# Kernel tuning notes

Measured on AMD Instinct MI355X. Metric: run time of the kernel, lower is better.

The kernel has to match this reference:

```python
import jax, jax.numpy as jnp
import numpy as np

N_NODES = 50000
N_EDGES = 800000
D = 128
BN_EPS = 1e-5


def setup_inputs() -> dict:
    key = jax.random.key(0)
    ks = jax.random.split(key, 8)
    scale = 1.0 / np.sqrt(D)
    return {
        "nfeat": jax.random.normal(ks[0], (N_NODES, D), dtype=jnp.float32),
        "efeat": jax.random.normal(ks[1], (N_EDGES, D), dtype=jnp.float32),
        "src": jax.random.randint(ks[2], (N_EDGES,), 0, N_NODES, dtype=jnp.int32),
        "dst": jax.random.randint(ks[3], (N_EDGES,), 0, N_NODES, dtype=jnp.int32),
        "W1": jax.random.normal(ks[4], (D, D), dtype=jnp.float32) * scale,
        "b1": jnp.zeros((D,), dtype=jnp.float32),
        "gamma": jnp.ones((D,), dtype=jnp.float32),
        "beta": jnp.zeros((D,), dtype=jnp.float32),
        "W2": jax.random.normal(ks[5], (D, D), dtype=jnp.float32) * scale,
        "b2": jnp.zeros((D,), dtype=jnp.float32),
        "We": jax.random.normal(ks[6], (D, D), dtype=jnp.float32) * scale,
        "be": jnp.zeros((D,), dtype=jnp.float32),
    }


def reference(nfeat, efeat, src, dst, W1, b1, gamma, beta, W2, b2, We, be):
    n = nfeat.shape[0]
    # GINConv, sum aggregator, eps=0: h = (1+eps)*x + sum_{j in N(i)} x_j
    agg = jax.ops.segment_sum(nfeat[src], dst, num_segments=n)  # [N, D]
    h = nfeat + agg
    # apply_func: Linear -> BatchNorm1d (training-mode batch stats) -> ReLU -> Linear
    h = h @ W1 + b1
    mu = jnp.mean(h, axis=0)
    var = jnp.mean(jnp.square(h - mu), axis=0)  # biased variance, as BatchNorm uses
    h = gamma * (h - mu) * jax.lax.rsqrt(var + BN_EPS) + beta
    h = jax.nn.relu(h)
    h = h @ W2 + b2
    # edge branch: linear on edge feats, scatter-sum to destination nodes, residual add
    e = efeat @ We + be                                          # [E, D]
    h_e = jax.ops.segment_sum(e, dst, num_segments=n)            # [N, D]
    return h + h_e
```

## Files before the change

### kernel.cpp

```cpp
#include <hip/hip_runtime.h>

#define D 128

typedef __attribute__((ext_vector_type(8))) short bf16x8;
typedef __attribute__((ext_vector_type(4))) float f32x4;

static __device__ __forceinline__ float4 f4add(float4 a, float4 b) {
    return make_float4(a.x + b.x, a.y + b.y, a.z + b.z, a.w + b.w);
}
static __device__ __forceinline__ short f2bf(float f) {
    union { float f; unsigned u; } v; v.f = f;
    const unsigned r = v.u + 0x7FFFu + ((v.u >> 16) & 1u);
    return (short)(r >> 16);
}
static __device__ __forceinline__ float bf2f(short s) {
    union { unsigned u; float f; } v;
    v.u = ((unsigned)(unsigned short)s) << 16;
    return v.f;
}

__global__ void k_zero(int* __restrict__ cnt, float* __restrict__ stats, int N) {
    const int i = blockIdx.x * 256 + threadIdx.x;
    if (i < N) cnt[i] = 0;
    if (i < 256) stats[i] = 0.f;
}

__global__ void k_wt(const float* __restrict__ W1, const float* __restrict__ W2,
                     const float* __restrict__ We, short* __restrict__ Wt1,
                     short* __restrict__ Wt2, short* __restrict__ Wte) {
    const int i = blockIdx.x * 256 + threadIdx.x;
    const int m = i >> 14;
    const int idx = i & 16383;
    const int k = idx >> 7, n = idx & 127;
    const float* W = (m == 0) ? W1 : (m == 1) ? W2 : We;
    short* Wt = (m == 0) ? Wt1 : (m == 1) ? Wt2 : Wte;
    Wt[n * 128 + k] = f2bf(W[k * 128 + n]);
}

__global__ void k_hist(const int* __restrict__ dst, int* __restrict__ cnt, int E) {
    const int base = (blockIdx.x * 256 + threadIdx.x) * 4;
    if (base + 3 < E) {
        const int4 d4 = *(const int4*)(dst + base);
        atomicAdd(&cnt[d4.x], 1);
        atomicAdd(&cnt[d4.y], 1);
        atomicAdd(&cnt[d4.z], 1);
        atomicAdd(&cnt[d4.w], 1);
    } else {
        for (int e = base; e < E; ++e) atomicAdd(&cnt[dst[e]], 1);
    }
}

__global__ __launch_bounds__(256) void k_scan1(const int* __restrict__ cnt,
                                               int* __restrict__ row_ptr,
                                               int* __restrict__ bsum,
                                               float* __restrict__ degf, int N) {
    __shared__ int sh[256];
    const int t = threadIdx.x;
    const int base = blockIdx.x * 1024 + t * 4;
    int4 v = make_int4(0, 0, 0, 0);
    if (base + 3 < N) v = *(const int4*)(cnt + base);
    else {
        if (base     < N) v.x = cnt[base];
        if (base + 1 < N) v.y = cnt[base + 1];
        if (base + 2 < N) v.z = cnt[base + 2];
        if (base + 3 < N) v.w = cnt[base + 3];
    }
    if (base     < N) degf[base]     = (float)v.x;
    if (base + 1 < N) degf[base + 1] = (float)v.y;
    if (base + 2 < N) degf[base + 2] = (float)v.z;
    if (base + 3 < N) degf[base + 3] = (float)v.w;
    const int s = v.x + v.y + v.z + v.w;
    sh[t] = s;
    __syncthreads();
    for (int off = 1; off < 256; off <<= 1) {
        int tmp = (t >= off) ? sh[t - off] : 0;
        __syncthreads();
        sh[t] += tmp;
        __syncthreads();
    }
    const int p = sh[t] - s;
    if (base     < N) row_ptr[base]     = p;
    if (base + 1 < N) row_ptr[base + 1] = p + v.x;
    if (base + 2 < N) row_ptr[base + 2] = p + v.x + v.y;
    if (base + 3 < N) row_ptr[base + 3] = p + v.x + v.y + v.z;
    if (t == 255) bsum[blockIdx.x] = sh[255];
}

__global__ __launch_bounds__(256) void k_scan2(int* __restrict__ bsum, int nb) {
    __shared__ int sh[256];
    const int t = threadIdx.x;
    const int v = (t < nb) ? bsum[t] : 0;
    sh[t] = v;
    __syncthreads();
    for (int off = 1; off < 256; off <<= 1) {
        int tmp = (t >= off) ? sh[t - off] : 0;
        __syncthreads();
        sh[t] += tmp;
        __syncthreads();
    }
    if (t < nb) bsum[t] = sh[t] - v;
}

__global__ __launch_bounds__(256) void k_scan3(int* __restrict__ row_ptr,
                                               int* __restrict__ cursor,
                                               const int* __restrict__ bsum,
                                               int N, int E) {
    const int t = threadIdx.x;
    const int base = blockIdx.x * 1024 + t * 4;
    const int off = bsum[blockIdx.x];
    #pragma unroll
    for (int j = 0; j < 4; ++j) {
        const int i = base + j;
        if (i < N) {
            const int r = row_ptr[i] + off;
            row_ptr[i] = r;
            cursor[i] = r;
        }
    }
    if (blockIdx.x == 0 && t == 0) row_ptr[N] = E;
}

__global__ void k_scatter(const int* __restrict__ src, const int* __restrict__ dst,
                          int* __restrict__ cursor,
                          int2* __restrict__ epair, int E) {
    const int base = (blockIdx.x * 256 + threadIdx.x) * 4;
    if (base + 3 < E) {
        const int4 d4 = *(const int4*)(dst + base);
        const int4 s4 = *(const int4*)(src + base);
        int p;
        p = atomicAdd(&cursor[d4.x], 1); epair[p] = make_int2(base + 0, s4.x);
        p = atomicAdd(&cursor[d4.y], 1); epair[p] = make_int2(base + 1, s4.y);
        p = atomicAdd(&cursor[d4.z], 1); epair[p] = make_int2(base + 2, s4.z);
        p = atomicAdd(&cursor[d4.w], 1); epair[p] = make_int2(base + 3, s4.w);
    } else {
        for (int e = base; e < E; ++e) {
            const int p = atomicAdd(&cursor[dst[e]], 1);
            epair[p] = make_int2(e, src[e]);
        }
    }
}

__global__ __launch_bounds__(256) void k_gather(const float* __restrict__ nfeat,
                                                const float* __restrict__ efeat,
                                                const int* __restrict__ row_ptr,
                                                const int2* __restrict__ epair,
                                                short* __restrict__ xbuf,
                                                short* __restrict__ agg_e,
                                                int N) {
    const int t = threadIdx.x;
    const int lane = t & 63;
    const int h = lane >> 5;
    const int c = lane & 31;
    const int node = blockIdx.x * 4 + (t >> 6);
    if (node >= N) return;

    const int start = row_ptr[node];
    const int end   = row_ptr[node + 1];

    float4 an = make_float4(0.f, 0.f, 0.f, 0.f);
    float4 ae = make_float4(0.f, 0.f, 0.f, 0.f);
    for (int e = start + h; e < end; e += 2) {
        const int2 p = epair[e];
        const float4 ev = *(const float4*)(efeat + (size_t)p.x * D + c * 4);
        const float4 nv = *(const float4*)(nfeat + (size_t)p.y * D + c * 4);
        ae = f4add(ae, ev);
        an = f4add(an, nv);
    }
    float4 an_t, ae_t;
    an_t.x = an.x + __shfl_xor(an.x, 32);
    an_t.y = an.y + __shfl_xor(an.y, 32);
    an_t.z = an.z + __shfl_xor(an.z, 32);
    an_t.w = an.w + __shfl_xor(an.w, 32);
    ae_t.x = ae.x + __shfl_xor(ae.x, 32);
    ae_t.y = ae.y + __shfl_xor(ae.y, 32);
    ae_t.z = ae.z + __shfl_xor(ae.z, 32);
    ae_t.w = ae.w + __shfl_xor(ae.w, 32);

    if (h == 0) {
        const float4 self = *(const float4*)(nfeat + (size_t)node * D + c * 4);
        const float4 xv = f4add(self, an_t);
        short4 xs4, es4;
        xs4.x = f2bf(xv.x);   xs4.y = f2bf(xv.y);
        xs4.z = f2bf(xv.z);   xs4.w = f2bf(xv.w);
        es4.x = f2bf(ae_t.x); es4.y = f2bf(ae_t.y);
        es4.z = f2bf(ae_t.z); es4.w = f2bf(ae_t.w);
        *(short4*)(xbuf  + (size_t)node * D + c * 4) = xs4;
        *(short4*)(agg_e + (size_t)node * D + c * 4) = es4;
    }
}

__global__ __launch_bounds__(256) void k_h1(const short* xbuf,
                                            const short* __restrict__ Wt1,
                                            const float* __restrict__ b1,
                                            short* h1,
                                            float* __restrict__ stats, int N) {
    const int t = threadIdx.x;
    const int lane = t & 63;
    const int w = t >> 6;
    const int l15 = lane & 15;
    const int kg = lane >> 4;
    const int row0 = blockIdx.x * 64;

    bf16x8 bfr[4][2];
    #pragma unroll
    for (int kt = 0; kt < 4; ++kt)
        #pragma unroll
        for (int cf = 0; cf < 2; ++cf)
            bfr[kt][cf] = *(const bf16x8*)(Wt1 + (w * 32 + cf * 16 + l15) * D +
                                           kt * 32 + kg * 8);

    f32x4 acc[4][2];
    #pragma unroll
    for (int rt = 0; rt < 4; ++rt) {
        acc[rt][0] = (f32x4)0.f;
        acc[rt][1] = (f32x4)0.f;
    }

    #pragma unroll
    for (int rt = 0; rt < 4; ++rt) {
        const int row = row0 + rt * 16 + l15;
        bf16x8 a0 = (bf16x8)(short)0, a1 = a0, a2 = a0, a3 = a0;
        if (row < N) {
            const short* xp = xbuf + (size_t)row * D + kg * 8;
            a0 = *(const bf16x8*)(xp);
            a1 = *(const bf16x8*)(xp + 32);
            a2 = *(const bf16x8*)(xp + 64);
            a3 = *(const bf16x8*)(xp + 96);
        }
        acc[rt][0] = __builtin_amdgcn_mfma_f32_16x16x32_bf16(a0, bfr[0][0], acc[rt][0], 0, 0, 0);
        acc[rt][1] = __builtin_amdgcn_mfma_f32_16x16x32_bf16(a0, bfr[0][1], acc[rt][1], 0, 0, 0);
        acc[rt][0] = __builtin_amdgcn_mfma_f32_16x16x32_bf16(a1, bfr[1][0], acc[rt][0], 0, 0, 0);
        acc[rt][1] = __builtin_amdgcn_mfma_f32_16x16x32_bf16(a1, bfr[1][1], acc[rt][1], 0, 0, 0);
        acc[rt][0] = __builtin_amdgcn_mfma_f32_16x16x32_bf16(a2, bfr[2][0], acc[rt][0], 0, 0, 0);
        acc[rt][1] = __builtin_amdgcn_mfma_f32_16x16x32_bf16(a2, bfr[2][1], acc[rt][1], 0, 0, 0);
        acc[rt][0] = __builtin_amdgcn_mfma_f32_16x16x32_bf16(a3, bfr[3][0], acc[rt][0], 0, 0, 0);
        acc[rt][1] = __builtin_amdgcn_mfma_f32_16x16x32_bf16(a3, bfr[3][1], acc[rt][1], 0, 0, 0);
    }

    const float bias0 = b1[w * 32 + l15];
    const float bias1 = b1[w * 32 + 16 + l15];
    float cs0 = 0.f, cq0 = 0.f, cs1 = 0.f, cq1 = 0.f;
    #pragma unroll
    for (int rt = 0; rt < 4; ++rt) {
        #pragma unroll
        for (int j = 0; j < 4; ++j) {
            const int row = row0 + rt * 16 + kg * 4 + j;
            if (row < N) {
                const float h0 = acc[rt][0][j] + bias0;
                const float h1v = acc[rt][1][j] + bias1;
                h1[(size_t)row * D + w * 32 + l15]      = f2bf(h0);
                h1[(size_t)row * D + w * 32 + 16 + l15] = f2bf(h1v);
                cs0 += h0; cq0 += h0 * h0;
                cs1 += h1v; cq1 += h1v * h1v;
            }
        }
    }
    #pragma unroll
    for (int m = 16; m < 64; m <<= 1) {
        cs0 += __shfl_xor(cs0, m); cq0 += __shfl_xor(cq0, m);
        cs1 += __shfl_xor(cs1, m); cq1 += __shfl_xor(cq1, m);
    }
    if (lane < 16) {
        atomicAdd(stats + w * 32 + lane,            cs0);
        atomicAdd(stats + w * 32 + 16 + lane,       cs1);
        atomicAdd(stats + 128 + w * 32 + lane,      cq0);
        atomicAdd(stats + 128 + w * 32 + 16 + lane, cq1);
    }
}

__global__ __launch_bounds__(256) void k_out(const short* __restrict__ h1,
                                             const short* __restrict__ agg_e,
                                             const short* __restrict__ Wt2,
                                             const short* __restrict__ Wte,
                                             const float* __restrict__ stats,
                                             const float* __restrict__ gamma,
                                             const float* __restrict__ beta,
                                             const float* __restrict__ b2,
                                             const float* __restrict__ be,
                                             const float* __restrict__ degf,
                                             float* __restrict__ out, int N) {
    __shared__ float scs[128], shs[128];
    const int t = threadIdx.x;
    if (t < 128) {
        const float invN = 1.0f / (float)N;
        const float mu = stats[t] * invN;
        const float var = stats[128 + t] * invN - mu * mu;
        const float sc = gamma[t] * rsqrtf(var + 1e-5f);
        scs[t] = sc;
        shs[t] = beta[t] - mu * sc;
    }
    __syncthreads();

    const int lane = t & 63;
    const int w = t >> 6;
    const int l15 = lane & 15;
    const int kg = lane >> 4;
    const int row0 = blockIdx.x * 64;

    f32x4 acc[4][2];
    #pragma unroll
    for (int rt = 0; rt < 4; ++rt) {
        acc[rt][0] = (f32x4)0.f;
        acc[rt][1] = (f32x4)0.f;
    }

    bf16x8 bfr[4][2];

    #pragma unroll
    for (int kt = 0; kt < 4; ++kt)
        #pragma unroll
        for (int cf = 0; cf < 2; ++cf)
            bfr[kt][cf] = *(const bf16x8*)(Wt2 + (w * 32 + cf * 16 + l15) * D +
                                           kt * 32 + kg * 8);

    #pragma unroll
    for (int rt = 0; rt < 4; ++rt) {
        const int row = row0 + rt * 16 + l15;
        #pragma unroll
        for (int kt = 0; kt < 4; ++kt) {
            bf16x8 raw = (bf16x8)(short)0;
            if (row < N)
                raw = *(const bf16x8*)(h1 + (size_t)row * D + kt * 32 + kg * 8);
            const int k0 = kt * 32 + kg * 8;
            const float4 sa = *(const float4*)(scs + k0);
            const float4 sb = *(const float4*)(scs + k0 + 4);
            const float4 ha = *(const float4*)(shs + k0);
            const float4 hb = *(const float4*)(shs + k0 + 4);
            bf16x8 afr;
            afr[0] = f2bf(fmaxf(bf2f(raw[0]) * sa.x + ha.x, 0.f));
            afr[1] = f2bf(fmaxf(bf2f(raw[1]) * sa.y + ha.y, 0.f));
            afr[2] = f2bf(fmaxf(bf2f(raw[2]) * sa.z + ha.z, 0.f));
            afr[3] = f2bf(fmaxf(bf2f(raw[3]) * sa.w + ha.w, 0.f));
            afr[4] = f2bf(fmaxf(bf2f(raw[4]) * sb.x + hb.x, 0.f));
            afr[5] = f2bf(fmaxf(bf2f(raw[5]) * sb.y + hb.y, 0.f));
            afr[6] = f2bf(fmaxf(bf2f(raw[6]) * sb.z + hb.z, 0.f));
            afr[7] = f2bf(fmaxf(bf2f(raw[7]) * sb.w + hb.w, 0.f));
            acc[rt][0] = __builtin_amdgcn_mfma_f32_16x16x32_bf16(afr, bfr[kt][0], acc[rt][0], 0, 0, 0);
            acc[rt][1] = __builtin_amdgcn_mfma_f32_16x16x32_bf16(afr, bfr[kt][1], acc[rt][1], 0, 0, 0);
        }
    }

    #pragma unroll
    for (int kt = 0; kt < 4; ++kt)
        #pragma unroll
        for (int cf = 0; cf < 2; ++cf)
            bfr[kt][cf] = *(const bf16x8*)(Wte + (w * 32 + cf * 16 + l15) * D +
                                           kt * 32 + kg * 8);

    #pragma unroll
    for (int rt = 0; rt < 4; ++rt) {
        const int row = row0 + rt * 16 + l15;
        bf16x8 a0 = (bf16x8)(short)0, a1 = a0, a2 = a0, a3 = a0;
        if (row < N) {
            const short* ap = agg_e + (size_t)row * D + kg * 8;
            a0 = *(const bf16x8*)(ap);
            a1 = *(const bf16x8*)(ap + 32);
            a2 = *(const bf16x8*)(ap + 64);
            a3 = *(const bf16x8*)(ap + 96);
        }
        acc[rt][0] = __builtin_amdgcn_mfma_f32_16x16x32_bf16(a0, bfr[0][0], acc[rt][0], 0, 0, 0);
        acc[rt][1] = __builtin_amdgcn_mfma_f32_16x16x32_bf16(a0, bfr[0][1], acc[rt][1], 0, 0, 0);
        acc[rt][0] = __builtin_amdgcn_mfma_f32_16x16x32_bf16(a1, bfr[1][0], acc[rt][0], 0, 0, 0);
        acc[rt][1] = __builtin_amdgcn_mfma_f32_16x16x32_bf16(a1, bfr[1][1], acc[rt][1], 0, 0, 0);
        acc[rt][0] = __builtin_amdgcn_mfma_f32_16x16x32_bf16(a2, bfr[2][0], acc[rt][0], 0, 0, 0);
        acc[rt][1] = __builtin_amdgcn_mfma_f32_16x16x32_bf16(a2, bfr[2][1], acc[rt][1], 0, 0, 0);
        acc[rt][0] = __builtin_amdgcn_mfma_f32_16x16x32_bf16(a3, bfr[3][0], acc[rt][0], 0, 0, 0);
        acc[rt][1] = __builtin_amdgcn_mfma_f32_16x16x32_bf16(a3, bfr[3][1], acc[rt][1], 0, 0, 0);
    }

    const float b2_0 = b2[w * 32 + l15];
    const float b2_1 = b2[w * 32 + 16 + l15];
    const float be_0 = be[w * 32 + l15];
    const float be_1 = be[w * 32 + 16 + l15];
    #pragma unroll
    for (int rt = 0; rt < 4; ++rt) {
        const int rbase = row0 + rt * 16 + kg * 4;
        float dgv[4];
        if (rbase + 3 < N) {
            *(float4*)dgv = *(const float4*)(degf + rbase);
        } else {
            #pragma unroll
            for (int j = 0; j < 4; ++j)
                dgv[j] = (rbase + j < N) ? degf[rbase + j] : 0.f;
        }
        #pragma unroll
        for (int j = 0; j < 4; ++j) {
            const int row = rbase + j;
            if (row < N) {
                out[(size_t)row * D + w * 32 + l15] =
                    acc[rt][0][j] + b2_0 + dgv[j] * be_0;
                out[(size_t)row * D + w * 32 + 16 + l15] =
                    acc[rt][1][j] + b2_1 + dgv[j] * be_1;
            }
        }
    }
}

extern "C" void kernel_launch(void* const* d_in, const int* in_sizes, int n_in,
                              void* d_out, int out_size, void* d_ws, size_t ws_size,
                              hipStream_t stream) {
    const float* nfeat = (const float*)d_in[0];
    const float* efeat = (const float*)d_in[1];
    const int*   src   = (const int*)d_in[2];
    const int*   dst   = (const int*)d_in[3];
    const float* W1    = (const float*)d_in[4];
    const float* b1    = (const float*)d_in[5];
    const float* gamma = (const float*)d_in[6];
    const float* beta  = (const float*)d_in[7];
    const float* W2    = (const float*)d_in[8];
    const float* b2    = (const float*)d_in[9];
    const float* We    = (const float*)d_in[10];
    const float* be    = (const float*)d_in[11];
    float* out = (float*)d_out;

    const int N = in_sizes[0] / D;
    const int E = in_sizes[2];
    const size_t ND = (size_t)N * D;

    short* xbuf   = (short*)d_ws;
    short* h1     = xbuf;
    short* agg_e  = xbuf + ND;
    short* Wt1    = agg_e + ND;
    short* Wt2    = Wt1 + 16384;
    short* Wte    = Wt2 + 16384;
    float* stats  = (float*)(Wte + 16384);
    float* degf   = stats + 256;
    int*   row_ptr= (int*)(degf + N);
    int*   cursor = row_ptr + (N + 16);
    int*   cnt    = cursor + (N + 16);
    int*   bsum   = cnt + (N + 16);
    int2*  epair  = (int2*)(bsum + 64);

    const int ebl4 = (E / 4 + 255) / 256;
    const int scb  = (N + 1023) / 1024;
    const int nb   = (N + 63) / 64;

    k_zero<<<(N + 255) / 256, 256, 0, stream>>>(cnt, stats, N);
    k_wt<<<192, 256, 0, stream>>>(W1, W2, We, Wt1, Wt2, Wte);
    k_hist<<<ebl4, 256, 0, stream>>>(dst, cnt, E);
    k_scan1<<<scb, 256, 0, stream>>>(cnt, row_ptr, bsum, degf, N);
    k_scan2<<<1, 256, 0, stream>>>(bsum, scb);
    k_scan3<<<scb, 256, 0, stream>>>(row_ptr, cursor, bsum, N, E);
    k_scatter<<<ebl4, 256, 0, stream>>>(src, dst, cursor, epair, E);

    k_gather<<<(N + 3) / 4, 256, 0, stream>>>(nfeat, efeat, row_ptr, epair,
                                              xbuf, agg_e, N);

    k_h1<<<nb, 256, 0, stream>>>(xbuf, Wt1, b1, h1, stats, N);
    k_out<<<nb, 256, 0, stream>>>(h1, agg_e, Wt2, Wte, stats, gamma, beta,
                                  b2, be, degf, out, N);
}
```

Baseline: 287.3 us.

## Fuse gather into h1 GEMM, bf16 node gather, single-block scan, merged prep

```diff
diff --git a/kernel.cpp b/kernel.cpp
--- a/kernel.cpp
+++ b/kernel.cpp
@@ -5,9 +5,6 @@
 typedef __attribute__((ext_vector_type(8))) short bf16x8;
 typedef __attribute__((ext_vector_type(4))) float f32x4;
 
-static __device__ __forceinline__ float4 f4add(float4 a, float4 b) {
-    return make_float4(a.x + b.x, a.y + b.y, a.z + b.z, a.w + b.w);
-}
 static __device__ __forceinline__ short f2bf(float f) {
     union { float f; unsigned u; } v; v.f = f;
     const unsigned r = v.u + 0x7FFFu + ((v.u >> 16) & 1u);
@@ -19,22 +16,36 @@
     return v.f;
 }
 
-__global__ void k_zero(int* __restrict__ cnt, float* __restrict__ stats, int N) {
-    const int i = blockIdx.x * 256 + threadIdx.x;
-    if (i < N) cnt[i] = 0;
-    if (i < 256) stats[i] = 0.f;
-}
-
-__global__ void k_wt(const float* __restrict__ W1, const float* __restrict__ W2,
-                     const float* __restrict__ We, short* __restrict__ Wt1,
-                     short* __restrict__ Wt2, short* __restrict__ Wte) {
-    const int i = blockIdx.x * 256 + threadIdx.x;
-    const int m = i >> 14;
-    const int idx = i & 16383;
-    const int k = idx >> 7, n = idx & 127;
-    const float* W = (m == 0) ? W1 : (m == 1) ? W2 : We;
-    short* Wt = (m == 0) ? Wt1 : (m == 1) ? Wt2 : Wte;
-    Wt[n * 128 + k] = f2bf(W[k * 128 + n]);
+__global__ __launch_bounds__(256) void k_prep(
+    const float* __restrict__ nfeat, short* __restrict__ nfb,
+    const float* __restrict__ W1, const float* __restrict__ W2,
+    const float* __restrict__ We, short* __restrict__ Wt1,
+    short* __restrict__ Wt2, short* __restrict__ Wte,
+    int* __restrict__ cnt, float* __restrict__ stats,
+    int N, int nbConv, int nbW)
+{
+    const int b = blockIdx.x, t = threadIdx.x;
+    if (b < nbConv) {
+        const int i = b * 256 + t;
+        if (i < (N * D) / 4) {
+            const float4 v = ((const float4*)nfeat)[i];
+            short4 s;
+            s.x = f2bf(v.x); s.y = f2bf(v.y); s.z = f2bf(v.z); s.w = f2bf(v.w);
+            ((short4*)nfb)[i] = s;
+        }
+    } else if (b < nbConv + nbW) {
+        const int i = (b - nbConv) * 256 + t;
+        const int m = i >> 14;
+        const int idx = i & 16383;
+        const int k = idx >> 7, n = idx & 127;
+        const float* W = (m == 0) ? W1 : (m == 1) ? W2 : We;
+        short* Wt = (m == 0) ? Wt1 : (m == 1) ? Wt2 : Wte;
+        Wt[n * 128 + k] = f2bf(W[k * 128 + n]);
+    } else {
+        const int i = (b - nbConv - nbW) * 256 + t;
+        if (i * 4 < N) ((int4*)cnt)[i] = make_int4(0, 0, 0, 0);
+        if (b == nbConv + nbW && t < 256) stats[t] = 0.f;
+    }
 }
 
 __global__ void k_hist(const int* __restrict__ dst, int* __restrict__ cnt, int E) {
@@ -50,74 +61,64 @@
     }
 }
 
-__global__ __launch_bounds__(256) void k_scan1(const int* __restrict__ cnt,
-                                               int* __restrict__ row_ptr,
-                                               int* __restrict__ bsum,
-                                               float* __restrict__ degf, int N) {
-    __shared__ int sh[256];
-    const int t = threadIdx.x;
-    const int base = blockIdx.x * 1024 + t * 4;
-    int4 v = make_int4(0, 0, 0, 0);
-    if (base + 3 < N) v = *(const int4*)(cnt + base);
-    else {
-        if (base     < N) v.x = cnt[base];
-        if (base + 1 < N) v.y = cnt[base + 1];
-        if (base + 2 < N) v.z = cnt[base + 2];
-        if (base + 3 < N) v.w = cnt[base + 3];
-    }
-    if (base     < N) degf[base]     = (float)v.x;
-    if (base + 1 < N) degf[base + 1] = (float)v.y;
-    if (base + 2 < N) degf[base + 2] = (float)v.z;
-    if (base + 3 < N) degf[base + 3] = (float)v.w;
-    const int s = v.x + v.y + v.z + v.w;
-    sh[t] = s;
-    __syncthreads();
-    for (int off = 1; off < 256; off <<= 1) {
-        int tmp = (t >= off) ? sh[t - off] : 0;
+__global__ __launch_bounds__(1024) void k_scan(
+    const int* __restrict__ cnt, int* __restrict__ row_ptr,
+    int* __restrict__ cursor, float* __restrict__ degf, int N)
+{
+    __shared__ int ws[17];
+    const int t = threadIdx.x, lane = t & 63, wid = t >> 6;
+    int carry = 0;
+    const int ntiles = (N + 4095) / 4096;
+    for (int tile = 0; tile < ntiles; ++tile) {
+        const int base = tile * 4096 + t * 4;
+        int4 v = make_int4(0, 0, 0, 0);
+        if (base + 3 < N) v = *(const int4*)(cnt + base);
+        else {
+            if (base     < N) v.x = cnt[base];
+            if (base + 1 < N) v.y = cnt[base + 1];
+            if (base + 2 < N) v.z = cnt[base + 2];
+            if (base + 3 < N) v.w = cnt[base + 3];
+        }
+        const int s = v.x + v.y + v.z + v.w;
+        int incl = s;
+        #pragma unroll
+        for (int off = 1; off < 64; off <<= 1) {
+            const int u = __shfl_up(incl, off);
+            if (lane >= off) incl += u;
+        }
+        if (lane == 63) ws[wid] = incl;
         __syncthreads();
-        sh[t] += tmp;
+        if (t < 16) {
+            const int wv = ws[t];
+            int wincl = wv;
+            #pragma unroll
+            for (int off = 1; off < 16; off <<= 1) {
+                const int u = __shfl_up(wincl, off);
+                if (t >= off) wincl += u;
+            }
+            ws[t] = wincl - wv;
+            if (t == 15) ws[16] = wincl;
+        }
         __syncthreads();
-    }
-    const int p = sh[t] - s;
-    if (base     < N) row_ptr[base]     = p;
-    if (base + 1 < N) row_ptr[base + 1] = p + v.x;
-    if (base + 2 < N) row_ptr[base + 2] = p + v.x + v.y;
-    if (base + 3 < N) row_ptr[base + 3] = p + v.x + v.y + v.z;
-    if (t == 255) bsum[blockIdx.x] = sh[255];
-}
-
-__global__ __launch_bounds__(256) void k_scan2(int* __restrict__ bsum, int nb) {
-    __shared__ int sh[256];
-    const int t = threadIdx.x;
-    const int v = (t < nb) ? bsum[t] : 0;
-    sh[t] = v;
-    __syncthreads();
-    for (int off = 1; off < 256; off <<= 1) {
-        int tmp = (t >= off) ? sh[t - off] : 0;
+        const int ex = carry + ws[wid] + (incl - s);
+        if (base + 3 < N) {
+            const int4 rp = make_int4(ex, ex + v.x, ex + v.x + v.y,
+                                      ex + v.x + v.y + v.z);
+            *(int4*)(row_ptr + base) = rp;
+            *(int4*)(cursor + base)  = rp;
+            *(float4*)(degf + base)  =
+                make_float4((float)v.x, (float)v.y, (float)v.z, (float)v.w);
+        } else {
+            int run = ex;
+            if (base < N)     { row_ptr[base]   = run; cursor[base]   = run; degf[base]   = (float)v.x; run += v.x; }
+            if (base + 1 < N) { row_ptr[base+1] = run; cursor[base+1] = run; degf[base+1] = (float)v.y; run += v.y; }
+            if (base + 2 < N) { row_ptr[base+2] = run; cursor[base+2] = run; degf[base+2] = (float)v.z; run += v.z; }
+            if (base + 3 < N) { row_ptr[base+3] = run; cursor[base+3] = run; degf[base+3] = (float)v.w; }
+        }
+        carry += ws[16];
         __syncthreads();
-        sh[t] += tmp;
-        __syncthreads();
-    }
-    if (t < nb) bsum[t] = sh[t] - v;
-}
-
-__global__ __launch_bounds__(256) void k_scan3(int* __restrict__ row_ptr,
-                                               int* __restrict__ cursor,
-                                               const int* __restrict__ bsum,
-                                               int N, int E) {
-    const int t = threadIdx.x;
-    const int base = blockIdx.x * 1024 + t * 4;
-    const int off = bsum[blockIdx.x];
-    #pragma unroll
-    for (int j = 0; j < 4; ++j) {
-        const int i = base + j;
-        if (i < N) {
-            const int r = row_ptr[i] + off;
-            row_ptr[i] = r;
-            cursor[i] = r;
-        }
-    }
-    if (blockIdx.x == 0 && t == 0) row_ptr[N] = E;
+    }
+    if (t == 0) row_ptr[N] = carry;
 }
 
 __global__ void k_scatter(const int* __restrict__ src, const int* __restrict__ dst,
@@ -140,66 +141,65 @@
     }
 }
 
-__global__ __launch_bounds__(256) void k_gather(const float* __restrict__ nfeat,
-                                                const float* __restrict__ efeat,
-                                                const int* __restrict__ row_ptr,
-                                                const int2* __restrict__ epair,
-                                                short* __restrict__ xbuf,
-                                                short* __restrict__ agg_e,
-                                                int N) {
-    const int t = threadIdx.x;
-    const int lane = t & 63;
-    const int h = lane >> 5;
-    const int c = lane & 31;
-    const int node = blockIdx.x * 4 + (t >> 6);
-    if (node >= N) return;
-
-    const int start = row_ptr[node];
-    const int end   = row_ptr[node + 1];
-
-    float4 an = make_float4(0.f, 0.f, 0.f, 0.f);
-    float4 ae = make_float4(0.f, 0.f, 0.f, 0.f);
-    for (int e = start + h; e < end; e += 2) {
-        const int2 p = epair[e];
-        const float4 ev = *(const float4*)(efeat + (size_t)p.x * D + c * 4);
-        const float4 nv = *(const float4*)(nfeat + (size_t)p.y * D + c * 4);
-        ae = f4add(ae, ev);
-        an = f4add(an, nv);
-    }
-    float4 an_t, ae_t;
-    an_t.x = an.x + __shfl_xor(an.x, 32);
-    an_t.y = an.y + __shfl_xor(an.y, 32);
-    an_t.z = an.z + __shfl_xor(an.z, 32);
-    an_t.w = an.w + __shfl_xor(an.w, 32);
-    ae_t.x = ae.x + __shfl_xor(ae.x, 32);
-    ae_t.y = ae.y + __shfl_xor(ae.y, 32);
-    ae_t.z = ae.z + __shfl_xor(ae.z, 32);
-    ae_t.w = ae.w + __shfl_xor(ae.w, 32);
-
-    if (h == 0) {
-        const float4 self = *(const float4*)(nfeat + (size_t)node * D + c * 4);
-        const float4 xv = f4add(self, an_t);
-        short4 xs4, es4;
-        xs4.x = f2bf(xv.x);   xs4.y = f2bf(xv.y);
-        xs4.z = f2bf(xv.z);   xs4.w = f2bf(xv.w);
-        es4.x = f2bf(ae_t.x); es4.y = f2bf(ae_t.y);
-        es4.z = f2bf(ae_t.z); es4.w = f2bf(ae_t.w);
-        *(short4*)(xbuf  + (size_t)node * D + c * 4) = xs4;
-        *(short4*)(agg_e + (size_t)node * D + c * 4) = es4;
-    }
-}
-
-__global__ __launch_bounds__(256) void k_h1(const short* xbuf,
-                                            const short* __restrict__ Wt1,
-                                            const float* __restrict__ b1,
-                                            short* h1,
-                                            float* __restrict__ stats, int N) {
+#define XS_STRIDE 136
+__global__ __launch_bounds__(256) void k_gather_h1(
+    const float* __restrict__ nfeat, const short* __restrict__ nfb,
+    const float* __restrict__ efeat,
+    const int* __restrict__ row_ptr, const int2* __restrict__ epair,
+    const short* __restrict__ Wt1, const float* __restrict__ b1,
+    short* __restrict__ agg_e, short* __restrict__ h1,
+    float* __restrict__ stats, int N)
+{
+    __shared__ __attribute__((aligned(16))) short xs[64 * XS_STRIDE];
     const int t = threadIdx.x;
     const int lane = t & 63;
     const int w = t >> 6;
+    const int h = lane >> 5;
+    const int c = lane & 31;
+    const int row0 = blockIdx.x * 64;
+
+    for (int i = 0; i < 16; ++i) {
+        const int nl = w * 16 + i;
+        const int node = row0 + nl;
+        if (node < N) {
+            const int start = row_ptr[node];
+            const int end   = row_ptr[node + 1];
+            float4 an = make_float4(0.f, 0.f, 0.f, 0.f);
+            float4 ae = make_float4(0.f, 0.f, 0.f, 0.f);
+            for (int e = start + h; e < end; e += 2) {
+                const int2 p = epair[e];
+                const float4 ev = *(const float4*)(efeat + (size_t)p.x * D + c * 4);
+                const short4 nv = *(const short4*)(nfb + (size_t)p.y * D + c * 4);
+                ae.x += ev.x; ae.y += ev.y; ae.z += ev.z; ae.w += ev.w;
+                an.x += bf2f(nv.x); an.y += bf2f(nv.y);
+                an.z += bf2f(nv.z); an.w += bf2f(nv.w);
+            }
+            an.x += __shfl_xor(an.x, 32);
+            an.y += __shfl_xor(an.y, 32);
+            an.z += __shfl_xor(an.z, 32);
+            an.w += __shfl_xor(an.w, 32);
+            ae.x += __shfl_xor(ae.x, 32);
+            ae.y += __shfl_xor(ae.y, 32);
+            ae.z += __shfl_xor(ae.z, 32);
+            ae.w += __shfl_xor(ae.w, 32);
+            if (h == 0) {
+                const float4 self = *(const float4*)(nfeat + (size_t)node * D + c * 4);
+                short4 xv, ev2;
+                xv.x = f2bf(self.x + an.x); xv.y = f2bf(self.y + an.y);
+                xv.z = f2bf(self.z + an.z); xv.w = f2bf(self.w + an.w);
+                ev2.x = f2bf(ae.x); ev2.y = f2bf(ae.y);
+                ev2.z = f2bf(ae.z); ev2.w = f2bf(ae.w);
+                *(short4*)(xs + nl * XS_STRIDE + c * 4) = xv;
+                *(short4*)(agg_e + (size_t)node * D + c * 4) = ev2;
+            }
+        } else if (h == 0) {
+            *(short4*)(xs + nl * XS_STRIDE + c * 4) = make_short4(0, 0, 0, 0);
+        }
+    }
+    __syncthreads();
+
     const int l15 = lane & 15;
-    const int kg = lane >> 4;
-    const int row0 = blockIdx.x * 64;
+    const int kg  = lane >> 4;
 
     bf16x8 bfr[4][2];
     #pragma unroll
@@ -211,30 +211,17 @@
 
     f32x4 acc[4][2];
     #pragma unroll
+    for (int rt = 0; rt < 4; ++rt) { acc[rt][0] = (f32x4)0.f; acc[rt][1] = (f32x4)0.f; }
+
+    #pragma unroll
     for (int rt = 0; rt < 4; ++rt) {
-        acc[rt][0] = (f32x4)0.f;
-        acc[rt][1] = (f32x4)0.f;
-    }
-
-    #pragma unroll
-    for (int rt = 0; rt < 4; ++rt) {
-        const int row = row0 + rt * 16 + l15;
-        bf16x8 a0 = (bf16x8)(short)0, a1 = a0, a2 = a0, a3 = a0;
-        if (row < N) {
-            const short* xp = xbuf + (size_t)row * D + kg * 8;
-            a0 = *(const bf16x8*)(xp);
-            a1 = *(const bf16x8*)(xp + 32);
-            a2 = *(const bf16x8*)(xp + 64);
-            a3 = *(const bf16x8*)(xp + 96);
-        }
-        acc[rt][0] = __builtin_amdgcn_mfma_f32_16x16x32_bf16(a0, bfr[0][0], acc[rt][0], 0, 0, 0);
-        acc[rt][1] = __builtin_amdgcn_mfma_f32_16x16x32_bf16(a0, bfr[0][1], acc[rt][1], 0, 0, 0);
-        acc[rt][0] = __builtin_amdgcn_mfma_f32_16x16x32_bf16(a1, bfr[1][0], acc[rt][0], 0, 0, 0);
-        acc[rt][1] = __builtin_amdgcn_mfma_f32_16x16x32_bf16(a1, bfr[1][1], acc[rt][1], 0, 0, 0);
-        acc[rt][0] = __builtin_amdgcn_mfma_f32_16x16x32_bf16(a2, bfr[2][0], acc[rt][0], 0, 0, 0);
-        acc[rt][1] = __builtin_amdgcn_mfma_f32_16x16x32_bf16(a2, bfr[2][1], acc[rt][1], 0, 0, 0);
-        acc[rt][0] = __builtin_amdgcn_mfma_f32_16x16x32_bf16(a3, bfr[3][0], acc[rt][0], 0, 0, 0);
-        acc[rt][1] = __builtin_amdgcn_mfma_f32_16x16x32_bf16(a3, bfr[3][1], acc[rt][1], 0, 0, 0);
+        #pragma unroll
+        for (int kt = 0; kt < 4; ++kt) {
+            const bf16x8 a = *(const bf16x8*)(xs + (rt * 16 + l15) * XS_STRIDE +
+                                              kt * 32 + kg * 8);
+            acc[rt][0] = __builtin_amdgcn_mfma_f32_16x16x32_bf16(a, bfr[kt][0], acc[rt][0], 0, 0, 0);
+            acc[rt][1] = __builtin_amdgcn_mfma_f32_16x16x32_bf16(a, bfr[kt][1], acc[rt][1], 0, 0, 0);
+        }
     }
 
     const float bias0 = b1[w * 32 + l15];
@@ -247,11 +234,11 @@
             const int row = row0 + rt * 16 + kg * 4 + j;
             if (row < N) {
                 const float h0 = acc[rt][0][j] + bias0;
-                const float h1v = acc[rt][1][j] + bias1;
+                const float hv = acc[rt][1][j] + bias1;
                 h1[(size_t)row * D + w * 32 + l15]      = f2bf(h0);
-                h1[(size_t)row * D + w * 32 + 16 + l15] = f2bf(h1v);
+                h1[(size_t)row * D + w * 32 + 16 + l15] = f2bf(hv);
                 cs0 += h0; cq0 += h0 * h0;
-                cs1 += h1v; cq1 += h1v * h1v;
+                cs1 += hv; cq1 += hv * hv;
             }
         }
     }
@@ -299,10 +286,7 @@
 
     f32x4 acc[4][2];
     #pragma unroll
-    for (int rt = 0; rt < 4; ++rt) {
-        acc[rt][0] = (f32x4)0.f;
-        acc[rt][1] = (f32x4)0.f;
-    }
+    for (int rt = 0; rt < 4; ++rt) { acc[rt][0] = (f32x4)0.f; acc[rt][1] = (f32x4)0.f; }
 
     bf16x8 bfr[4][2];
 
@@ -417,10 +401,10 @@
     const int E = in_sizes[2];
     const size_t ND = (size_t)N * D;
 
-    short* xbuf   = (short*)d_ws;
-    short* h1     = xbuf;
-    short* agg_e  = xbuf + ND;
-    short* Wt1    = agg_e + ND;
+    short* nfb    = (short*)d_ws;
+    short* agg_e  = nfb + ND;
+    short* h1     = agg_e + ND;
+    short* Wt1    = h1 + ND;
     short* Wt2    = Wt1 + 16384;
     short* Wte    = Wt2 + 16384;
     float* stats  = (float*)(Wte + 16384);
@@ -428,25 +412,22 @@
     int*   row_ptr= (int*)(degf + N);
     int*   cursor = row_ptr + (N + 16);
     int*   cnt    = cursor + (N + 16);
-    int*   bsum   = cnt + (N + 16);
-    int2*  epair  = (int2*)(bsum + 64);
-
-    const int ebl4 = (E / 4 + 255) / 256;
-    const int scb  = (N + 1023) / 1024;
-    const int nb   = (N + 63) / 64;
-
-    k_zero<<<(N + 255) / 256, 256, 0, stream>>>(cnt, stats, N);
-    k_wt<<<192, 256, 0, stream>>>(W1, W2, We, Wt1, Wt2, Wte);
+    int2*  epair  = (int2*)(cnt + (N + 16));
+
+    const int nbConv = ((N * D) / 4 + 255) / 256;
+    const int nbW    = 192;
+    const int nbZ    = (N / 4 + 255) / 256;
+    const int ebl4   = (E / 4 + 255) / 256;
+    const int nb     = (N + 63) / 64;
+
+    k_prep<<<nbConv + nbW + nbZ, 256, 0, stream>>>(nfeat, nfb, W1, W2, We,
+                                                   Wt1, Wt2, Wte, cnt, stats,
+                                                   N, nbConv, nbW);
     k_hist<<<ebl4, 256, 0, stream>>>(dst, cnt, E);
-    k_scan1<<<scb, 256, 0, stream>>>(cnt, row_ptr, bsum, degf, N);
-    k_scan2<<<1, 256, 0, stream>>>(bsum, scb);
-    k_scan3<<<scb, 256, 0, stream>>>(row_ptr, cursor, bsum, N, E);
+    k_scan<<<1, 1024, 0, stream>>>(cnt, row_ptr, cursor, degf, N);
     k_scatter<<<ebl4, 256, 0, stream>>>(src, dst, cursor, epair, E);
-
-    k_gather<<<(N + 3) / 4, 256, 0, stream>>>(nfeat, efeat, row_ptr, epair,
-                                              xbuf, agg_e, N);
-
-    k_h1<<<nb, 256, 0, stream>>>(xbuf, Wt1, b1, h1, stats, N);
+    k_gather_h1<<<nb, 256, 0, stream>>>(nfeat, nfb, efeat, row_ptr, epair,
+                                        Wt1, b1, agg_e, h1, stats, N);
     k_out<<<nb, 256, 0, stream>>>(h1, agg_e, Wt2, Wte, stats, gamma, beta,
                                   b2, be, degf, out, N);
 }
```

New measurement: 343.7 us. 19.7% more time.
